# Performance work log

Measured on AMD Instinct MI355X. Metric: run time of the kernel, lower is better.

Reference implementation:

```python
import jax, jax.numpy as jnp
import numpy as np

F = 16      # frames
NV = 4096   # visual points per frame
NT = 512    # tactile points per frame
M = 4096    # model points
SCALE = 0.1


def setup_inputs() -> dict:
    key = jax.random.key(0)
    ks = jax.random.split(key, 6)
    return {
        "state": jax.random.normal(ks[0], (6,), dtype=jnp.float32) * 0.1,
        "model_points": jax.random.normal(ks[1], (M, 3), dtype=jnp.float32),
        "visual_points": jax.random.normal(ks[2], (F, NV, 3), dtype=jnp.float32),
        "tactile_points": jax.random.normal(ks[3], (F, NT, 3), dtype=jnp.float32),
        "physics_pred_states": jax.random.normal(ks[4], (F, 12), dtype=jnp.float32) * 0.1,
        "delta_time": jax.random.uniform(ks[5], (F,), dtype=jnp.float32, minval=0.01, maxval=0.05),
    }


def _skew(a):
    z = jnp.zeros((), a.dtype)
    return jnp.array([[z, -a[2], a[1]],
                      [a[2], z, -a[0]],
                      [-a[1], a[0], z]])


def _rot_from_omega(omega, dt):
    # Rodrigues: R = I + sin(theta*dt) S + (1 - cos(theta*dt)) S@S, S = skew(omega/|omega|)
    theta = jnp.linalg.norm(omega)
    ax = omega / jnp.clip(theta, 1e-8)
    S = _skew(ax)
    return jnp.eye(3, dtype=omega.dtype) + jnp.sin(theta * dt) * S + (1.0 - jnp.cos(theta * dt)) * (S @ S)


def _chamfer(pred, gt):
    # rows: pred [N,3], cols: gt [M,3]; row-min of squared distances, then mean
    d = (jnp.sum(pred * pred, axis=1)[:, None]
         + jnp.sum(gt * gt, axis=1)[None, :]
         - 2.0 * pred @ gt.T)
    return jnp.mean(jnp.min(d, axis=1))


def reference(state, model_points, visual_points, tactile_points, physics_pred_states, delta_time):
    t0 = state[:3]
    r0 = _rot_from_omega(state[3:], jnp.float32(1.0))  # Euler2Mat modeled as axis-angle

    def pose_step(carry, x):
        t, r = carry
        v, omega, dt = x
        t = t + v * dt
        r = _rot_from_omega(omega, dt) @ r
        return (t, r), (t, r)

    _, (ts, rs) = jax.lax.scan(
        pose_step, (t0, r0),
        (physics_pred_states[1:, 6:9], physics_pred_states[1:, 9:12], delta_time[1:]))
    ts = jnp.concatenate([t0[None], ts], axis=0)  # [F,3]
    rs = jnp.concatenate([r0[None], rs], axis=0)  # [F,3,3]

    def frame_loss(acc, x):
        t, r, vp, tp = x
        vc = ((vp - t) @ r) / SCALE
        tc = ((tp - t) @ r) / SCALE
        acc = acc + _chamfer(vc, model_points) + 0.1 * _chamfer(tc, model_points)
        return acc, None

    E_cd, _ = jax.lax.scan(frame_loss, jnp.zeros((), jnp.float32),
                           (ts, rs, visual_points, tactile_points))
    return E_cd
```

## Files before the change

### kernel.cpp

```cpp
#include <hip/hip_runtime.h>
#include <math.h>

#define F_    16
#define NV_   4096
#define NT_   512
#define M_    4096
#define PPF_  (NV_ + NT_)
#define NPTS_ (F_ * PPF_)
#define SCALE_INV 10.0f

#define TPB   256
#define PTSB  96
#define NBLK  (NPTS_ / PTSB)
#define NMG   8
#define MPG   (M_ / NMG)
#define CHM   64
#define NCH   (MPG / CHM)
#define FS    66
#define PPL   3

__device__ inline void rot_from_omega(float ox, float oy, float oz, float dt,
                                      float* R) {
    float theta = sqrtf(ox * ox + oy * oy + oz * oz);
    float inv = 1.0f / fmaxf(theta, 1e-8f);
    float ax = ox * inv, ay = oy * inv, az = oz * inv;
    float s = sinf(theta * dt);
    float c = 1.0f - cosf(theta * dt);
    R[0] = 1.0f - c * (ay * ay + az * az);
    R[1] = -s * az + c * ax * ay;
    R[2] =  s * ay + c * ax * az;
    R[3] =  s * az + c * ax * ay;
    R[4] = 1.0f - c * (ax * ax + az * az);
    R[5] = -s * ax + c * ay * az;
    R[6] = -s * ay + c * ax * az;
    R[7] =  s * ax + c * ay * az;
    R[8] = 1.0f - c * (ax * ax + ay * ay);
}

__global__ __launch_bounds__(TPB) void chamfer_one(
    const float* __restrict__ state, const float* __restrict__ model,
    const float* __restrict__ vis, const float* __restrict__ tac,
    const float* __restrict__ phys, const float* __restrict__ dts,
    float* __restrict__ out) {
    __shared__ float4 featD[2][NMG * FS];
    __shared__ float  sposes[F_ * 12];
    __shared__ float  sRs[F_ * 9];
    __shared__ float  sdt[F_ * 3];
    __shared__ float  sdm[PTSB][NMG + 1];
    __shared__ float  sw[2];

    const int t = threadIdx.x;

    if (t < F_) {
        float ox, oy, oz, dt;
        if (t == 0) { ox = state[3]; oy = state[4]; oz = state[5]; dt = 1.0f; }
        else        { ox = phys[t * 12 + 9]; oy = phys[t * 12 + 10];
                      oz = phys[t * 12 + 11]; dt = dts[t]; }
        float Rs[9];
        rot_from_omega(ox, oy, oz, dt, Rs);
        for (int j = 0; j < 9; ++j) sRs[t * 9 + j] = Rs[j];
        if (t > 0) {
            sdt[t * 3 + 0] = phys[t * 12 + 6] * dt;
            sdt[t * 3 + 1] = phys[t * 12 + 7] * dt;
            sdt[t * 3 + 2] = phys[t * 12 + 8] * dt;
        }
    }
    if (t == 0) {
        float R[9];
        for (int j = 0; j < 9; ++j) R[j] = sRs[j];
        float tr[3] = {state[0], state[1], state[2]};
        for (int i = 0; i < F_; ++i) {
            if (i > 0) {
                tr[0] += sdt[i * 3 + 0];
                tr[1] += sdt[i * 3 + 1];
                tr[2] += sdt[i * 3 + 2];
                float Rn[9];
                const float* Rsp = sRs + i * 9;
                for (int r = 0; r < 3; ++r)
                    for (int c2 = 0; c2 < 3; ++c2)
                        Rn[r * 3 + c2] = Rsp[r * 3 + 0] * R[0 + c2] +
                                         Rsp[r * 3 + 1] * R[3 + c2] +
                                         Rsp[r * 3 + 2] * R[6 + c2];
                for (int j = 0; j < 9; ++j) R[j] = Rn[j];
            }
            float* o = sposes + i * 12;
            o[0] = tr[0]; o[1] = tr[1]; o[2] = tr[2];
            for (int j = 0; j < 9; ++j) o[3 + j] = R[j] * SCALE_INV;
        }
    }

    {
        const int g = t >> 5, m = t & 31;
        int id = g * MPG + m;
        float gx = model[id * 3 + 0], gy = model[id * 3 + 1], gz = model[id * 3 + 2];
        featD[0][g * FS + m] = make_float4(-2.0f * gx, -2.0f * gy, -2.0f * gz,
                                           gx * gx + gy * gy + gz * gz);
        id += 32;
        gx = model[id * 3 + 0]; gy = model[id * 3 + 1]; gz = model[id * 3 + 2];
        featD[0][g * FS + m + 32] = make_float4(-2.0f * gx, -2.0f * gy, -2.0f * gz,
                                                gx * gx + gy * gy + gz * gz);
    }
    __syncthreads();

    const int pl = t & 31;
    const int mg = t >> 5;
    const int f = (blockIdx.x * PTSB) / PPF_;
    const int lbase = blockIdx.x * PTSB - f * PPF_;

    float c0[PPL], c1[PPL], c2[PPL], cn[PPL], dm[PPL];
    {
        const float* ps = sposes + f * 12;
#pragma unroll
        for (int k = 0; k < PPL; ++k) {
            int loc = lbase + k * 32 + pl;
            const float* p = (loc < NV_) ? (vis + ((size_t)f * NV_ + loc) * 3)
                                         : (tac + ((size_t)f * NT_ + (loc - NV_)) * 3);
            float px = p[0], py = p[1], pz = p[2];
            float d0 = px - ps[0], d1 = py - ps[1], d2 = pz - ps[2];
            const float* R = ps + 3;
            float x = d0 * R[0] + d1 * R[3] + d2 * R[6];
            float y = d0 * R[1] + d1 * R[4] + d2 * R[7];
            float z = d0 * R[2] + d1 * R[5] + d2 * R[8];
            c0[k] = x; c1[k] = y; c2[k] = z;
            cn[k] = x * x + y * y + z * z;
            dm[k] = 3.4e38f;
        }
    }

    for (int c = 0; c < NCH; ++c) {
        const int cur = c & 1;
        if (c + 1 < NCH) {
            const int g = t >> 5, m = t & 31;
            int id = g * MPG + (c + 1) * CHM + m;
            float gx = model[id * 3 + 0], gy = model[id * 3 + 1], gz = model[id * 3 + 2];
            featD[cur ^ 1][g * FS + m] = make_float4(-2.0f * gx, -2.0f * gy, -2.0f * gz,
                                                     gx * gx + gy * gy + gz * gz);
            id += 32;
            gx = model[id * 3 + 0]; gy = model[id * 3 + 1]; gz = model[id * 3 + 2];
            featD[cur ^ 1][g * FS + m + 32] = make_float4(-2.0f * gx, -2.0f * gy, -2.0f * gz,
                                                          gx * gx + gy * gy + gz * gz);
        }
        const float4* fb = &featD[cur][mg * FS];
#pragma unroll
        for (int m = 0; m < CHM; m += 2) {
            float4 ga = fb[m];
            float4 gb = fb[m + 1];
#pragma unroll
            for (int k = 0; k < PPL; ++k) {
                float da = fmaf(ga.x, c0[k], fmaf(ga.y, c1[k], fmaf(ga.z, c2[k], ga.w)));
                float db = fmaf(gb.x, c0[k], fmaf(gb.y, c1[k], fmaf(gb.z, c2[k], gb.w)));
                dm[k] = fminf(dm[k], fminf(da, db));
            }
        }
        __syncthreads();
    }

#pragma unroll
    for (int k = 0; k < PPL; ++k) sdm[k * 32 + pl][mg] = dm[k] + cn[k];
    __syncthreads();

    float v = 0.0f;
    if (t < PTSB) {
        float mn = sdm[t][0];
#pragma unroll
        for (int i = 1; i < NMG; ++i) mn = fminf(mn, sdm[t][i]);
        const int loc = lbase + t;
        const float w = (loc < NV_) ? (1.0f / NV_) : (0.1f / NT_);
        v = mn * w;
    }
    if (t < 128) {
#pragma unroll
        for (int off = 32; off > 0; off >>= 1) v += __shfl_down(v, off);
        if ((t & 63) == 0) sw[t >> 6] = v;
    }
    __syncthreads();
    if (t == 0) atomicAdd(out, sw[0] + sw[1]);
}

extern "C" void kernel_launch(void* const* d_in, const int* in_sizes, int n_in,
                              void* d_out, int out_size, void* d_ws, size_t ws_size,
                              hipStream_t stream) {
    const float* state = (const float*)d_in[0];
    const float* model = (const float*)d_in[1];
    const float* vis   = (const float*)d_in[2];
    const float* tac   = (const float*)d_in[3];
    const float* phys  = (const float*)d_in[4];
    const float* dts   = (const float*)d_in[5];
    float* out = (float*)d_out;
    (void)d_ws; (void)ws_size;

    hipMemsetAsync(out, 0, sizeof(float), stream);
    chamfer_one<<<NBLK, TPB, 0, stream>>>(state, model, vis, tac, phys, dts, out);
}
```

Measured before the change: 101.3 us.

## Precompute poses and model features in a prep kernel, register-block with packed FMA

Moves the pose chain and model feature construction into a separate prep kernel that writes to workspace. The main kernel now keeps 18 query points per thread in registers and splits the model points into 64 groups of 16-point chunks. Distances are computed with inline-asm v_pk_fma_f32 so two points are handled per instruction. Per-block redundant pose and feature work goes away and arithmetic intensity per LDS load rises, at the cost of an extra launch, a large cross-group min reduction in LDS, and higher register pressure; a slow fallback kernel is used if the workspace is too small.

```diff
diff --git a/kernel.cpp b/kernel.cpp
--- a/kernel.cpp
+++ b/kernel.cpp
@@ -10,14 +10,17 @@
 #define SCALE_INV 10.0f
 
 #define TPB   256
-#define PTSB  96
+#define PTSB  72
 #define NBLK  (NPTS_ / PTSB)
-#define NMG   8
-#define MPG   (M_ / NMG)
-#define CHM   64
+#define NG    64
+#define MPG   (M_ / NG)
+#define CHM   16
 #define NCH   (MPG / CHM)
-#define FS    66
-#define PPL   3
+#define FG    68
+#define PPL   18
+#define NPR   9
+
+typedef float v2f __attribute__((ext_vector_type(2)));
 
 __device__ inline void rot_from_omega(float ox, float oy, float oz, float dt,
                                       float* R) {
@@ -37,144 +40,239 @@
     R[8] = 1.0f - c * (ax * ax + ay * ay);
 }
 
-__global__ __launch_bounds__(TPB) void chamfer_one(
+__device__ __forceinline__ void dist6(v2f qa01, v2f qa23, v2f qb01, v2f qb23,
+                                      v2f c0a, v2f c0b, v2f c0c,
+                                      v2f c1a, v2f c1b, v2f c1c,
+                                      v2f c2a, v2f c2b, v2f c2c, float* dmp) {
+    v2f A0, A1, A2, B0, B1, B2;
+    asm("v_pk_fma_f32 %0, %7, %16, %7 op_sel:[0,0,1] op_sel_hi:[0,1,1]\n\t"
+        "v_pk_fma_f32 %1, %7, %17, %7 op_sel:[0,0,1] op_sel_hi:[0,1,1]\n\t"
+        "v_pk_fma_f32 %2, %7, %18, %7 op_sel:[0,0,1] op_sel_hi:[0,1,1]\n\t"
+        "v_pk_fma_f32 %3, %9, %16, %9 op_sel:[0,0,1] op_sel_hi:[0,1,1]\n\t"
+        "v_pk_fma_f32 %4, %9, %17, %9 op_sel:[0,0,1] op_sel_hi:[0,1,1]\n\t"
+        "v_pk_fma_f32 %5, %9, %18, %9 op_sel:[0,0,1] op_sel_hi:[0,1,1]\n\t"
+        "v_pk_fma_f32 %0, %6, %13, %0 op_sel:[1,0,0] op_sel_hi:[1,1,1]\n\t"
+        "v_pk_fma_f32 %1, %6, %14, %1 op_sel:[1,0,0] op_sel_hi:[1,1,1]\n\t"
+        "v_pk_fma_f32 %2, %6, %15, %2 op_sel:[1,0,0] op_sel_hi:[1,1,1]\n\t"
+        "v_pk_fma_f32 %3, %8, %13, %3 op_sel:[1,0,0] op_sel_hi:[1,1,1]\n\t"
+        "v_pk_fma_f32 %4, %8, %14, %4 op_sel:[1,0,0] op_sel_hi:[1,1,1]\n\t"
+        "v_pk_fma_f32 %5, %8, %15, %5 op_sel:[1,0,0] op_sel_hi:[1,1,1]\n\t"
+        "v_pk_fma_f32 %0, %6, %10, %0 op_sel:[0,0,0] op_sel_hi:[0,1,1]\n\t"
+        "v_pk_fma_f32 %1, %6, %11, %1 op_sel:[0,0,0] op_sel_hi:[0,1,1]\n\t"
+        "v_pk_fma_f32 %2, %6, %12, %2 op_sel:[0,0,0] op_sel_hi:[0,1,1]\n\t"
+        "v_pk_fma_f32 %3, %8, %10, %3 op_sel:[0,0,0] op_sel_hi:[0,1,1]\n\t"
+        "v_pk_fma_f32 %4, %8, %11, %4 op_sel:[0,0,0] op_sel_hi:[0,1,1]\n\t"
+        "v_pk_fma_f32 %5, %8, %12, %5 op_sel:[0,0,0] op_sel_hi:[0,1,1]"
+        : "=&v"(A0), "=&v"(A1), "=&v"(A2), "=&v"(B0), "=&v"(B1), "=&v"(B2)
+        : "v"(qa01), "v"(qa23), "v"(qb01), "v"(qb23),
+          "v"(c0a), "v"(c0b), "v"(c0c),
+          "v"(c1a), "v"(c1b), "v"(c1c),
+          "v"(c2a), "v"(c2b), "v"(c2c));
+    dmp[0] = fminf(fminf(A0.x, B0.x), dmp[0]);
+    dmp[1] = fminf(fminf(A0.y, B0.y), dmp[1]);
+    dmp[2] = fminf(fminf(A1.x, B1.x), dmp[2]);
+    dmp[3] = fminf(fminf(A1.y, B1.y), dmp[3]);
+    dmp[4] = fminf(fminf(A2.x, B2.x), dmp[4]);
+    dmp[5] = fminf(fminf(A2.y, B2.y), dmp[5]);
+}
+
+__global__ void prep_kernel(const float* __restrict__ state,
+                            const float* __restrict__ phys,
+                            const float* __restrict__ dts,
+                            const float* __restrict__ model,
+                            float* __restrict__ ws_pose,
+                            float4* __restrict__ ws_feat) {
+    const int b = blockIdx.x, t = threadIdx.x;
+    if (b == 0) {
+        __shared__ float sRs[F_ * 9];
+        __shared__ float sdt[F_ * 3];
+        if (t < F_) {
+            float ox, oy, oz, dt;
+            if (t == 0) { ox = state[3]; oy = state[4]; oz = state[5]; dt = 1.0f; }
+            else        { ox = phys[t * 12 + 9]; oy = phys[t * 12 + 10];
+                          oz = phys[t * 12 + 11]; dt = dts[t]; }
+            float Rs[9];
+            rot_from_omega(ox, oy, oz, dt, Rs);
+            for (int j = 0; j < 9; ++j) sRs[t * 9 + j] = Rs[j];
+            if (t > 0) {
+                sdt[t * 3 + 0] = phys[t * 12 + 6] * dt;
+                sdt[t * 3 + 1] = phys[t * 12 + 7] * dt;
+                sdt[t * 3 + 2] = phys[t * 12 + 8] * dt;
+            }
+        }
+        if (t == 0) {
+            float R[9];
+            for (int j = 0; j < 9; ++j) R[j] = sRs[j];
+            float tr[3] = {state[0], state[1], state[2]};
+            for (int i = 0; i < F_; ++i) {
+                if (i > 0) {
+                    tr[0] += sdt[i * 3 + 0];
+                    tr[1] += sdt[i * 3 + 1];
+                    tr[2] += sdt[i * 3 + 2];
+                    float Rn[9];
+                    const float* Rsp = sRs + i * 9;
+                    for (int r = 0; r < 3; ++r)
+                        for (int c2 = 0; c2 < 3; ++c2)
+                            Rn[r * 3 + c2] = Rsp[r * 3 + 0] * R[0 + c2] +
+                                             Rsp[r * 3 + 1] * R[3 + c2] +
+                                             Rsp[r * 3 + 2] * R[6 + c2];
+                    for (int j = 0; j < 9; ++j) R[j] = Rn[j];
+                }
+                float* o = ws_pose + i * 12;
+                o[0] = tr[0]; o[1] = tr[1]; o[2] = tr[2];
+                for (int j = 0; j < 9; ++j) o[3 + j] = R[j] * SCALE_INV;
+            }
+        }
+    } else {
+        const int id = (b - 1) * 256 + t;
+        float gx = model[id * 3 + 0], gy = model[id * 3 + 1], gz = model[id * 3 + 2];
+        const int c = (id >> 4) & 3, g = id >> 6, m = id & 15;
+        ws_feat[c * 1024 + g * 16 + m] =
+            make_float4(-2.0f * gx, -2.0f * gy, -2.0f * gz,
+                        gx * gx + gy * gy + gz * gz);
+    }
+}
+
+__global__ __launch_bounds__(TPB, 4) void chamfer_main(
+    const float* __restrict__ vis, const float* __restrict__ tac,
+    const float* __restrict__ ws_pose, const float4* __restrict__ ws_feat,
+    float* __restrict__ out) {
+    __shared__ float4 feat[CHM * FG];
+    __shared__ float  sdm2[NG * 80];
+    __shared__ float  spose[F_ * 12];
+    __shared__ float  sw[4];
+
+    const int t  = threadIdx.x;
+    const int g  = t >> 2;
+    const int pl = t & 3;
+    const int f  = blockIdx.x >> 6;
+    const int lbase = (blockIdx.x & 63) * PTSB;
+
+    if (t < F_ * 12) spose[t] = ws_pose[t];
+#pragma unroll
+    for (int j = 0; j < 4; ++j) {
+        int flat = t + 256 * j;
+        feat[(flat & 15) * FG + (flat >> 4)] = ws_feat[flat];
+    }
+    __syncthreads();
+
+    float Rr[9], trx, try_, trz;
+    {
+        const float* ps = spose + f * 12;
+        trx = ps[0]; try_ = ps[1]; trz = ps[2];
+        for (int j = 0; j < 9; ++j) Rr[j] = ps[3 + j];
+    }
+
+    v2f c0p[NPR], c1p[NPR], c2p[NPR];
+    float cn[PPL], dm[PPL];
+#pragma unroll
+    for (int k = 0; k < PPL; ++k) {
+        int loc = lbase + pl * PPL + k;
+        const float* p = (loc < NV_) ? (vis + ((size_t)f * NV_ + loc) * 3)
+                                     : (tac + ((size_t)f * NT_ + (loc - NV_)) * 3);
+        float d0 = p[0] - trx, d1 = p[1] - try_, d2 = p[2] - trz;
+        float x = d0 * Rr[0] + d1 * Rr[3] + d2 * Rr[6];
+        float y = d0 * Rr[1] + d1 * Rr[4] + d2 * Rr[7];
+        float z = d0 * Rr[2] + d1 * Rr[5] + d2 * Rr[8];
+        cn[k] = x * x + y * y + z * z;
+        dm[k] = 3.4e38f;
+        if (k & 1) { c0p[k >> 1].y = x; c1p[k >> 1].y = y; c2p[k >> 1].y = z; }
+        else       { c0p[k >> 1].x = x; c1p[k >> 1].x = y; c2p[k >> 1].x = z; }
+    }
+
+    for (int c = 0;; ++c) {
+#pragma unroll 2
+        for (int m = 0; m < CHM; m += 2) {
+            float4 ga = feat[m * FG + g];
+            float4 gb = feat[(m + 1) * FG + g];
+            v2f qa01 = (v2f){ga.x, ga.y}, qa23 = (v2f){ga.z, ga.w};
+            v2f qb01 = (v2f){gb.x, gb.y}, qb23 = (v2f){gb.z, gb.w};
+            dist6(qa01, qa23, qb01, qb23, c0p[0], c0p[1], c0p[2],
+                  c1p[0], c1p[1], c1p[2], c2p[0], c2p[1], c2p[2], dm);
+            dist6(qa01, qa23, qb01, qb23, c0p[3], c0p[4], c0p[5],
+                  c1p[3], c1p[4], c1p[5], c2p[3], c2p[4], c2p[5], dm + 6);
+            dist6(qa01, qa23, qb01, qb23, c0p[6], c0p[7], c0p[8],
+                  c1p[6], c1p[7], c1p[8], c2p[6], c2p[7], c2p[8], dm + 12);
+        }
+        if (c == NCH - 1) break;
+        __syncthreads();
+#pragma unroll
+        for (int j = 0; j < 4; ++j) {
+            int flat = t + 256 * j;
+            feat[(flat & 15) * FG + (flat >> 4)] = ws_feat[(c + 1) * 1024 + flat];
+        }
+        __syncthreads();
+    }
+
+    {
+        float* seg = &sdm2[g * 80 + pl * 20];
+#pragma unroll
+        for (int k = 0; k < PPL; ++k) seg[k] = dm[k] + cn[k];
+    }
+    __syncthreads();
+
+    float v = 0.0f;
+    if (t < PTSB) {
+        const int off = t + 2 * (t / 18);
+        float mn = sdm2[off];
+#pragma unroll 8
+        for (int i = 1; i < NG; ++i) mn = fminf(mn, sdm2[i * 80 + off]);
+        const int loc = lbase + t;
+        const float w = (loc < NV_) ? (1.0f / NV_) : (0.1f / NT_);
+        v = mn * w;
+    }
+#pragma unroll
+    for (int off2 = 32; off2 > 0; off2 >>= 1) v += __shfl_down(v, off2);
+    if ((t & 63) == 0) sw[t >> 6] = v;
+    __syncthreads();
+    if (t == 0) atomicAdd(out, sw[0] + sw[1] + sw[2] + sw[3]);
+}
+
+__global__ __launch_bounds__(TPB) void chamfer_fb(
     const float* __restrict__ state, const float* __restrict__ model,
     const float* __restrict__ vis, const float* __restrict__ tac,
     const float* __restrict__ phys, const float* __restrict__ dts,
     float* __restrict__ out) {
-    __shared__ float4 featD[2][NMG * FS];
-    __shared__ float  sposes[F_ * 12];
-    __shared__ float  sRs[F_ * 9];
-    __shared__ float  sdt[F_ * 3];
-    __shared__ float  sdm[PTSB][NMG + 1];
-    __shared__ float  sw[2];
-
-    const int t = threadIdx.x;
-
-    if (t < F_) {
-        float ox, oy, oz, dt;
-        if (t == 0) { ox = state[3]; oy = state[4]; oz = state[5]; dt = 1.0f; }
-        else        { ox = phys[t * 12 + 9]; oy = phys[t * 12 + 10];
-                      oz = phys[t * 12 + 11]; dt = dts[t]; }
-        float Rs[9];
-        rot_from_omega(ox, oy, oz, dt, Rs);
-        for (int j = 0; j < 9; ++j) sRs[t * 9 + j] = Rs[j];
-        if (t > 0) {
-            sdt[t * 3 + 0] = phys[t * 12 + 6] * dt;
-            sdt[t * 3 + 1] = phys[t * 12 + 7] * dt;
-            sdt[t * 3 + 2] = phys[t * 12 + 8] * dt;
-        }
-    }
-    if (t == 0) {
-        float R[9];
-        for (int j = 0; j < 9; ++j) R[j] = sRs[j];
-        float tr[3] = {state[0], state[1], state[2]};
-        for (int i = 0; i < F_; ++i) {
-            if (i > 0) {
-                tr[0] += sdt[i * 3 + 0];
-                tr[1] += sdt[i * 3 + 1];
-                tr[2] += sdt[i * 3 + 2];
-                float Rn[9];
-                const float* Rsp = sRs + i * 9;
-                for (int r = 0; r < 3; ++r)
-                    for (int c2 = 0; c2 < 3; ++c2)
-                        Rn[r * 3 + c2] = Rsp[r * 3 + 0] * R[0 + c2] +
-                                         Rsp[r * 3 + 1] * R[3 + c2] +
-                                         Rsp[r * 3 + 2] * R[6 + c2];
-                for (int j = 0; j < 9; ++j) R[j] = Rn[j];
-            }
-            float* o = sposes + i * 12;
-            o[0] = tr[0]; o[1] = tr[1]; o[2] = tr[2];
-            for (int j = 0; j < 9; ++j) o[3 + j] = R[j] * SCALE_INV;
-        }
-    }
-
-    {
-        const int g = t >> 5, m = t & 31;
-        int id = g * MPG + m;
-        float gx = model[id * 3 + 0], gy = model[id * 3 + 1], gz = model[id * 3 + 2];
-        featD[0][g * FS + m] = make_float4(-2.0f * gx, -2.0f * gy, -2.0f * gz,
-                                           gx * gx + gy * gy + gz * gz);
-        id += 32;
-        gx = model[id * 3 + 0]; gy = model[id * 3 + 1]; gz = model[id * 3 + 2];
-        featD[0][g * FS + m + 32] = make_float4(-2.0f * gx, -2.0f * gy, -2.0f * gz,
-                                                gx * gx + gy * gy + gz * gz);
-    }
+    __shared__ float sw[4];
+    const int pt = blockIdx.x * TPB + threadIdx.x;
+    const int f = pt / PPF_, loc = pt - f * PPF_;
+    float R[9], tr[3] = {state[0], state[1], state[2]};
+    rot_from_omega(state[3], state[4], state[5], 1.0f, R);
+    for (int i = 1; i <= f; ++i) {
+        float dt = dts[i];
+        tr[0] += phys[i * 12 + 6] * dt;
+        tr[1] += phys[i * 12 + 7] * dt;
+        tr[2] += phys[i * 12 + 8] * dt;
+        float Rs[9], Rn[9];
+        rot_from_omega(phys[i * 12 + 9], phys[i * 12 + 10], phys[i * 12 + 11], dt, Rs);
+        for (int r = 0; r < 3; ++r)
+            for (int c2 = 0; c2 < 3; ++c2)
+                Rn[r * 3 + c2] = Rs[r * 3 + 0] * R[0 + c2] +
+                                 Rs[r * 3 + 1] * R[3 + c2] +
+                                 Rs[r * 3 + 2] * R[6 + c2];
+        for (int j = 0; j < 9; ++j) R[j] = Rn[j];
+    }
+    for (int j = 0; j < 9; ++j) R[j] *= SCALE_INV;
+    const float* p = (loc < NV_) ? (vis + ((size_t)f * NV_ + loc) * 3)
+                                 : (tac + ((size_t)f * NT_ + (loc - NV_)) * 3);
+    float d0 = p[0] - tr[0], d1 = p[1] - tr[1], d2 = p[2] - tr[2];
+    float x = d0 * R[0] + d1 * R[3] + d2 * R[6];
+    float y = d0 * R[1] + d1 * R[4] + d2 * R[7];
+    float z = d0 * R[2] + d1 * R[5] + d2 * R[8];
+    float cn = x * x + y * y + z * z;
+    float mn = 3.4e38f;
+    for (int i = 0; i < M_; ++i) {
+        float gx = model[i * 3], gy = model[i * 3 + 1], gz = model[i * 3 + 2];
+        float gn = gx * gx + gy * gy + gz * gz;
+        float dd = fmaf(-2.0f * gx, x, fmaf(-2.0f * gy, y, fmaf(-2.0f * gz, z, gn)));
+        mn = fminf(mn, dd);
+    }
+    float w = (loc < NV_) ? (1.0f / NV_) : (0.1f / NT_);
+    float v = (mn + cn) * w;
+    for (int off = 32; off > 0; off >>= 1) v += __shfl_down(v, off);
+    if ((threadIdx.x & 63) == 0) sw[threadIdx.x >> 6] = v;
     __syncthreads();
-
-    const int pl = t & 31;
-    const int mg = t >> 5;
-    const int f = (blockIdx.x * PTSB) / PPF_;
-    const int lbase = blockIdx.x * PTSB - f * PPF_;
-
-    float c0[PPL], c1[PPL], c2[PPL], cn[PPL], dm[PPL];
-    {
-        const float* ps = sposes + f * 12;
-#pragma unroll
-        for (int k = 0; k < PPL; ++k) {
-            int loc = lbase + k * 32 + pl;
-            const float* p = (loc < NV_) ? (vis + ((size_t)f * NV_ + loc) * 3)
-                                         : (tac + ((size_t)f * NT_ + (loc - NV_)) * 3);
-            float px = p[0], py = p[1], pz = p[2];
-            float d0 = px - ps[0], d1 = py - ps[1], d2 = pz - ps[2];
-            const float* R = ps + 3;
-            float x = d0 * R[0] + d1 * R[3] + d2 * R[6];
-            float y = d0 * R[1] + d1 * R[4] + d2 * R[7];
-            float z = d0 * R[2] + d1 * R[5] + d2 * R[8];
-            c0[k] = x; c1[k] = y; c2[k] = z;
-            cn[k] = x * x + y * y + z * z;
-            dm[k] = 3.4e38f;
-        }
-    }
-
-    for (int c = 0; c < NCH; ++c) {
-        const int cur = c & 1;
-        if (c + 1 < NCH) {
-            const int g = t >> 5, m = t & 31;
-            int id = g * MPG + (c + 1) * CHM + m;
-            float gx = model[id * 3 + 0], gy = model[id * 3 + 1], gz = model[id * 3 + 2];
-            featD[cur ^ 1][g * FS + m] = make_float4(-2.0f * gx, -2.0f * gy, -2.0f * gz,
-                                                     gx * gx + gy * gy + gz * gz);
-            id += 32;
-            gx = model[id * 3 + 0]; gy = model[id * 3 + 1]; gz = model[id * 3 + 2];
-            featD[cur ^ 1][g * FS + m + 32] = make_float4(-2.0f * gx, -2.0f * gy, -2.0f * gz,
-                                                          gx * gx + gy * gy + gz * gz);
-        }
-        const float4* fb = &featD[cur][mg * FS];
-#pragma unroll
-        for (int m = 0; m < CHM; m += 2) {
-            float4 ga = fb[m];
-            float4 gb = fb[m + 1];
-#pragma unroll
-            for (int k = 0; k < PPL; ++k) {
-                float da = fmaf(ga.x, c0[k], fmaf(ga.y, c1[k], fmaf(ga.z, c2[k], ga.w)));
-                float db = fmaf(gb.x, c0[k], fmaf(gb.y, c1[k], fmaf(gb.z, c2[k], gb.w)));
-                dm[k] = fminf(dm[k], fminf(da, db));
-            }
-        }
-        __syncthreads();
-    }
-
-#pragma unroll
-    for (int k = 0; k < PPL; ++k) sdm[k * 32 + pl][mg] = dm[k] + cn[k];
-    __syncthreads();
-
-    float v = 0.0f;
-    if (t < PTSB) {
-        float mn = sdm[t][0];
-#pragma unroll
-        for (int i = 1; i < NMG; ++i) mn = fminf(mn, sdm[t][i]);
-        const int loc = lbase + t;
-        const float w = (loc < NV_) ? (1.0f / NV_) : (0.1f / NT_);
-        v = mn * w;
-    }
-    if (t < 128) {
-#pragma unroll
-        for (int off = 32; off > 0; off >>= 1) v += __shfl_down(v, off);
-        if ((t & 63) == 0) sw[t >> 6] = v;
-    }
-    __syncthreads();
-    if (t == 0) atomicAdd(out, sw[0] + sw[1]);
+    if (threadIdx.x == 0) atomicAdd(out, sw[0] + sw[1] + sw[2] + sw[3]);
 }
 
 extern "C" void kernel_launch(void* const* d_in, const int* in_sizes, int n_in,
@@ -187,8 +285,16 @@
     const float* phys  = (const float*)d_in[4];
     const float* dts   = (const float*)d_in[5];
     float* out = (float*)d_out;
-    (void)d_ws; (void)ws_size;
-
+
+    const size_t NEED = 1024 + (size_t)M_ * sizeof(float4);
     hipMemsetAsync(out, 0, sizeof(float), stream);
-    chamfer_one<<<NBLK, TPB, 0, stream>>>(state, model, vis, tac, phys, dts, out);
-}
+    if (ws_size >= NEED) {
+        float*  ws_pose = (float*)d_ws;
+        float4* ws_feat = (float4*)((char*)d_ws + 1024);
+        prep_kernel<<<17, 256, 0, stream>>>(state, phys, dts, model, ws_pose, ws_feat);
+        chamfer_main<<<NBLK, TPB, 0, stream>>>(vis, tac, ws_pose, ws_feat, out);
+    } else {
+        chamfer_fb<<<NPTS_ / TPB, TPB, 0, stream>>>(state, model, vis, tac, phys,
+                                                    dts, out);
+    }
+}
```

After: 101.5 us. About the same (+0.2%).
